# Performance work log

Hardware: AMD Instinct MI355X
Metric: run time of the kernel (lower is better)

## Reference

```python
import jax, jax.numpy as jnp
import numpy as np
import math

B, I, O, C = 8192, 1024, 1024, 6


def setup_inputs() -> dict:
    key = jax.random.key(0)
    k1, k2, k3, k4 = jax.random.split(key, 4)
    inputs = jax.random.normal(k1, (B, I), dtype=jnp.float32)
    phase_radians = jax.random.uniform(k2, (B,), dtype=jnp.float32) * (2.0 * math.pi)
    # xavier-uniform per control point: bound = sqrt(6/(I+O))
    bound = math.sqrt(6.0 / (I + O))
    weight_control_points = jax.random.uniform(k3, (C, O, I), dtype=jnp.float32, minval=-bound, maxval=bound)
    bias_control_points = jnp.zeros((C, O), dtype=jnp.float32) + 0.01 * jax.random.normal(k4, (C, O), dtype=jnp.float32)
    return {"inputs": inputs, "phase_radians": phase_radians,
            "weight_control_points": weight_control_points,
            "bias_control_points": bias_control_points}


def _catmull_rom(phase_radians, num_control_points):
    two_pi = 2.0 * math.pi
    phase = jnp.remainder(phase_radians, two_pi)
    position = phase * (float(num_control_points) / two_pi)
    base = jnp.floor(position)
    base_idx = base.astype(jnp.int32)
    t = position - base
    t2 = t * t
    t3 = t2 * t
    indices = jnp.stack([
        jnp.remainder(base_idx - 1, num_control_points),
        jnp.remainder(base_idx, num_control_points),
        jnp.remainder(base_idx + 1, num_control_points),
        jnp.remainder(base_idx + 2, num_control_points),
    ], axis=1)  # [B, 4]
    weights = jnp.stack([
        -0.5 * t + t2 - 0.5 * t3,
        1.0 - 2.5 * t2 + 1.5 * t3,
        0.5 * t + 2.0 * t2 - 1.5 * t3,
        -0.5 * t2 + 0.5 * t3,
    ], axis=1)  # [B, 4]
    return indices, weights


def reference(inputs, phase_radians, weight_control_points, bias_control_points):
    # Faithful to: out[b] = sum_k w[b,k] * (W[idx[b,k]] @ x[b] + bias[idx[b,k]])
    # Instead of materializing [B,O,I] interpolated weights, compute all C
    # control-point projections once and gather the 4 needed per sample.
    num_cp = weight_control_points.shape[0]
    indices, cr_weights = _catmull_rom(phase_radians.astype(inputs.dtype), num_cp)
    y_all = jnp.einsum('coi,bi->bco', weight_control_points, inputs)  # [B, C, O]
    y_sel = jnp.take_along_axis(y_all, indices[:, :, None], axis=1)  # [B, 4, O]
    b_sel = bias_control_points[indices]                              # [B, 4, O]
    return jnp.einsum('bk,bko->bo', cr_weights, y_sel + b_sel)
```

## Files before the change

kernel.cpp:

```cpp
#include <hip/hip_runtime.h>
#include <hip/hip_bf16.h>
#include <math.h>

#define B_SZ 8192
#define I_SZ 1024
#define O_SZ 1024
#define NCP  6

typedef __attribute__((ext_vector_type(8))) short bf16x8;
typedef __attribute__((ext_vector_type(4))) float f32x4;

__device__ __forceinline__ unsigned short f2bf(float f) {
  union { float f; unsigned int u; } v; v.f = f;
  unsigned int u = v.u;
  u += 0x7FFFu + ((u >> 16) & 1u);
  return (unsigned short)(u >> 16);
}

__global__ void cvt_f32_to_bf16(const float* __restrict__ src,
                                unsigned short* __restrict__ dst, int n4) {
  int idx = blockIdx.x * blockDim.x + threadIdx.x;
  int stride = gridDim.x * blockDim.x;
  for (int i = idx; i < n4; i += stride) {
    float4 v = reinterpret_cast<const float4*>(src)[i];
    ushort4 o;
    o.x = f2bf(v.x); o.y = f2bf(v.y); o.z = f2bf(v.z); o.w = f2bf(v.w);
    reinterpret_cast<ushort4*>(dst)[i] = o;
  }
}

__device__ __forceinline__ void gload_lds16(const void* g, void* l) {
  __builtin_amdgcn_global_load_lds(
      (const __attribute__((address_space(1))) void*)g,
      (__attribute__((address_space(3))) void*)l, 16, 0, 0);
}

#define BM 256
#define BN 128
#define BK 64
#define NT 96
#define NBUF 3

__global__ __launch_bounds__(512, 1) void pfl_gemm(
    const unsigned short* __restrict__ xb,
    const unsigned short* __restrict__ wb,
    const float* __restrict__ phase,
    const float* __restrict__ bias,
    float* __restrict__ out) {
  __shared__ __align__(16) unsigned short Abuf[NBUF][BM * BK];
  __shared__ __align__(16) unsigned short Bbuf[NBUF][BN * BK];
  __shared__ __align__(16) float c4[NCP][BM];

  const int nbn = O_SZ / BN;
  int bid = (int)blockIdx.x;
  int swz = (bid & 7) * 32 + (bid >> 3);
  int brow = (swz / nbn) * BM;
  int bcol = (swz % nbn) * BN;

  int tid = (int)threadIdx.x;
  int lane = tid & 63;
  int wid = tid >> 6;
  int wr = wid >> 1;
  int wc = wid & 1;

  if (tid < BM) {
    float ph = phase[brow + tid];
    const float two_pi = 6.2831855f;
    float pm = fmodf(ph, two_pi);
    float pos = pm * (float)(6.0 / 6.283185307179586);
    float base = floorf(pos);
    int bi = (int)base;
    float t = pos - base;
    float t2 = t * t, t3 = t2 * t;
    float w0 = -0.5f * t + t2 - 0.5f * t3;
    float w1 = 1.0f - 2.5f * t2 + 1.5f * t3;
    float w2 = 0.5f * t + 2.0f * t2 - 1.5f * t3;
    float w3 = -0.5f * t2 + 0.5f * t3;
    float cc[NCP] = {0.f, 0.f, 0.f, 0.f, 0.f, 0.f};
    cc[((bi - 1) % NCP + NCP) % NCP] += w0;
    cc[(bi % NCP + NCP) % NCP]       += w1;
    cc[((bi + 1) % NCP + NCP) % NCP] += w2;
    cc[((bi + 2) % NCP + NCP) % NCP] += w3;
    for (int j = 0; j < NCP; ++j) c4[j][tid] = cc[j];
  }

  f32x4 acc[4][4];
  f32x4 part[4][4];
#pragma unroll
  for (int m = 0; m < 4; ++m)
#pragma unroll
    for (int n = 0; n < 4; ++n) {
      acc[m][n] = (f32x4){0.f, 0.f, 0.f, 0.f};
      part[m][n] = (f32x4){0.f, 0.f, 0.f, 0.f};
    }

  int swzcol = ((lane & 7) ^ (lane >> 3)) * 8;
  const unsigned short* xsrc =
      xb + (size_t)(brow + wid * 8 + (lane >> 3)) * I_SZ + swzcol;
  const unsigned short* wsrc =
      wb + (size_t)(bcol + wid * 8 + (lane >> 3)) * I_SZ + swzcol;

  int lbase = (lane & 15) * 128 + (((lane >> 4) ^ (lane & 7)) & 7) * 16;

  auto STAGE = [&](int t, int b) {
    int ks = (t & 15) * 64;
    int j = t >> 4;
    const unsigned short* xs = xsrc + ks;
    const unsigned short* ws = wsrc + (size_t)j * O_SZ * I_SZ + ks;
    unsigned short* Ad = &Abuf[b][(wid * 8) * BK];
    unsigned short* Bd = &Bbuf[b][(wid * 8) * BK];
#pragma unroll
    for (int p = 0; p < 4; ++p)
      gload_lds16(xs + (size_t)p * 64 * I_SZ, Ad + p * 64 * BK);
#pragma unroll
    for (int p = 0; p < 2; ++p)
      gload_lds16(ws + (size_t)p * 64 * I_SZ, Bd + p * 64 * BK);
  };

  STAGE(0, 0);
  STAGE(1, 1);
  asm volatile("s_waitcnt vmcnt(6)" ::: "memory");
  __builtin_amdgcn_sched_barrier(0);
  __syncthreads();

  int cur = 0;
  for (int t = 0; t < NT; ++t) {
    const char* Ab = (const char*)&Abuf[cur][0];
    const char* Bb = (const char*)&Bbuf[cur][0];
    int st = cur + 2; if (st >= NBUF) st -= NBUF;

    bf16x8 af0[4], bf0[4], af1[4], bf1[4];
#pragma unroll
    for (int m = 0; m < 4; ++m)
      af0[m] = *reinterpret_cast<const bf16x8*>(
          Ab + (wr * 64 + m * 16) * 128 + lbase);
#pragma unroll
    for (int n = 0; n < 4; ++n)
      bf0[n] = *reinterpret_cast<const bf16x8*>(
          Bb + (wc * 64 + n * 16) * 128 + lbase);
    if (t + 2 < NT) STAGE(t + 2, st);
    asm volatile("s_waitcnt lgkmcnt(0)" ::: "memory");
    __builtin_amdgcn_sched_barrier(0);

#pragma unroll
    for (int m = 0; m < 4; ++m)
      af1[m] = *reinterpret_cast<const bf16x8*>(
          Ab + (wr * 64 + m * 16) * 128 + (lbase ^ 64));
#pragma unroll
    for (int n = 0; n < 4; ++n)
      bf1[n] = *reinterpret_cast<const bf16x8*>(
          Bb + (wc * 64 + n * 16) * 128 + (lbase ^ 64));
    __builtin_amdgcn_sched_barrier(0);

    __builtin_amdgcn_s_setprio(1);
#pragma unroll
    for (int m = 0; m < 4; ++m)
#pragma unroll
      for (int n = 0; n < 4; ++n)
        part[m][n] = __builtin_amdgcn_mfma_f32_16x16x32_bf16(
            af0[m], bf0[n], part[m][n], 0, 0, 0);
    __builtin_amdgcn_s_setprio(0);

    asm volatile("s_waitcnt lgkmcnt(0)" ::: "memory");
    __builtin_amdgcn_sched_barrier(0);

    __builtin_amdgcn_s_setprio(1);
#pragma unroll
    for (int m = 0; m < 4; ++m)
#pragma unroll
      for (int n = 0; n < 4; ++n)
        part[m][n] = __builtin_amdgcn_mfma_f32_16x16x32_bf16(
            af1[m], bf1[n], part[m][n], 0, 0, 0);
    __builtin_amdgcn_s_setprio(0);

    if ((t & 15) == 15) {
      int j = t >> 4;
#pragma unroll
      for (int m = 0; m < 4; ++m) {
        f32x4 cv = *reinterpret_cast<const f32x4*>(
            &c4[j][wr * 64 + m * 16 + (lane >> 4) * 4]);
#pragma unroll
        for (int n = 0; n < 4; ++n) {
          acc[m][n] += cv * part[m][n];
          part[m][n] = (f32x4){0.f, 0.f, 0.f, 0.f};
        }
      }
    }

    if (t + 2 < NT)
      asm volatile("s_waitcnt vmcnt(6)" ::: "memory");
    else
      asm volatile("s_waitcnt vmcnt(0)" ::: "memory");
    __builtin_amdgcn_sched_barrier(0);
    __builtin_amdgcn_s_barrier();
    ++cur; if (cur == NBUF) cur = 0;
  }

#pragma unroll
  for (int n = 0; n < 4; ++n) {
    int col = bcol + wc * 64 + n * 16 + (lane & 15);
    float b6[NCP];
#pragma unroll
    for (int j = 0; j < NCP; ++j) b6[j] = bias[j * O_SZ + col];
#pragma unroll
    for (int m = 0; m < 4; ++m) {
#pragma unroll
      for (int r = 0; r < 4; ++r) {
        int rloc = wr * 64 + m * 16 + (lane >> 4) * 4 + r;
        float s = 0.f;
#pragma unroll
        for (int j = 0; j < NCP; ++j) s += c4[j][rloc] * b6[j];
        out[(size_t)(brow + rloc) * O_SZ + col] = acc[m][n][r] + s;
      }
    }
  }
}

extern "C" void kernel_launch(void* const* d_in, const int* in_sizes, int n_in,
                              void* d_out, int out_size, void* d_ws, size_t ws_size,
                              hipStream_t stream) {
  (void)in_sizes; (void)n_in; (void)out_size; (void)ws_size;
  const float* x     = (const float*)d_in[0];
  const float* phase = (const float*)d_in[1];
  const float* w     = (const float*)d_in[2];
  const float* bias  = (const float*)d_in[3];
  float* out = (float*)d_out;

  unsigned short* xb = (unsigned short*)d_ws;
  unsigned short* wb = (unsigned short*)((char*)d_ws +
                        (size_t)B_SZ * I_SZ * sizeof(unsigned short));

  cvt_f32_to_bf16<<<2048, 256, 0, stream>>>(x, xb, B_SZ * I_SZ / 4);
  cvt_f32_to_bf16<<<1536, 256, 0, stream>>>(w, wb, NCP * O_SZ * I_SZ / 4);

  dim3 grid((B_SZ / BM) * (O_SZ / BN));
  pfl_gemm<<<grid, 512, 0, stream>>>(xb, wb, phase, bias, out);
}
```

Measured before the change: 123.2 us.

## Sort rows by spline segment to skip unused control-point GEMMs

Adds a single-block counting sort that groups batch rows by their Catmull-Rom base segment, then permutes and casts x into sorted order. Each 256-row block now loops only over the contiguous range of control points its rows actually need (typically 4 instead of 6), cutting MFMA work and weight traffic. Output rows are scattered back through the permutation. The cost is an extra serial sort kernel with an O(256) prefix loop per thread, a gather-based cast, and scattered output writes.

```diff
diff --git a/kernel.cpp b/kernel.cpp
--- a/kernel.cpp
+++ b/kernel.cpp
@@ -29,6 +29,78 @@
   }
 }
 
+__device__ __forceinline__ int seg_of(float ph) {
+  const float two_pi = 6.2831855f;
+  const float scale = (float)(6.0 / 6.283185307179586);
+  float pm = fmodf(ph, two_pi);
+  int bi = (int)floorf(pm * scale);
+  return ((bi % NCP) + NCP) % NCP;
+}
+
+__global__ void sort_rows(const float* __restrict__ phase,
+                          unsigned short* __restrict__ perm,
+                          int* __restrict__ blkinfo) {
+  __shared__ int hist[256][NCP];
+  __shared__ int segtot[NCP];
+  __shared__ int cum[NCP + 1];
+  __shared__ int thrbase[256][NCP];
+  int t = (int)threadIdx.x;
+  for (int s = 0; s < NCP; ++s) hist[t][s] = 0;
+  for (int i = 0; i < 32; ++i) {
+    int b = t * 32 + i;
+    hist[t][seg_of(phase[b])]++;
+  }
+  __syncthreads();
+  if (t < NCP) {
+    int tot = 0;
+    for (int tt = 0; tt < 256; ++tt) tot += hist[tt][t];
+    segtot[t] = tot;
+  }
+  __syncthreads();
+  if (t == 0) {
+    cum[0] = 0;
+    for (int s = 0; s < NCP; ++s) cum[s + 1] = cum[s] + segtot[s];
+  }
+  __syncthreads();
+  for (int s = 0; s < NCP; ++s) {
+    int p = 0;
+    for (int tt = 0; tt < t; ++tt) p += hist[tt][s];
+    thrbase[t][s] = cum[s] + p;
+  }
+  for (int i = 0; i < 32; ++i) {
+    int b = t * 32 + i;
+    int s = seg_of(phase[b]);
+    int pos = thrbase[t][s]++;
+    perm[pos] = (unsigned short)b;
+  }
+  __syncthreads();
+  if (t < B_SZ / 256) {
+    int start = t * 256, end = start + 255;
+    int s0 = 0; while (s0 < NCP - 1 && cum[s0 + 1] <= start) ++s0;
+    int s1 = 0; while (s1 < NCP - 1 && cum[s1 + 1] <= end) ++s1;
+    int nj = s1 - s0 + 4; if (nj > NCP) nj = NCP;
+    blkinfo[2 * t] = (s0 + NCP - 1) % NCP;
+    blkinfo[2 * t + 1] = nj;
+  }
+}
+
+__global__ void cast_x_perm(const float* __restrict__ x,
+                            const unsigned short* __restrict__ perm,
+                            unsigned short* __restrict__ xb) {
+  int idx = blockIdx.x * blockDim.x + threadIdx.x;
+  int stride = gridDim.x * blockDim.x;
+  const int total = B_SZ * (I_SZ / 4);
+  for (int i = idx; i < total; i += stride) {
+    int pos = i >> 8;
+    int c = i & 255;
+    int src = (int)perm[pos];
+    float4 v = reinterpret_cast<const float4*>(x + (size_t)src * I_SZ)[c];
+    ushort4 o;
+    o.x = f2bf(v.x); o.y = f2bf(v.y); o.z = f2bf(v.z); o.w = f2bf(v.w);
+    reinterpret_cast<ushort4*>(xb + (size_t)pos * I_SZ)[c] = o;
+  }
+}
+
 __device__ __forceinline__ void gload_lds16(const void* g, void* l) {
   __builtin_amdgcn_global_load_lds(
       (const __attribute__((address_space(1))) void*)g,
@@ -38,23 +110,26 @@
 #define BM 256
 #define BN 128
 #define BK 64
-#define NT 96
 #define NBUF 3
 
 __global__ __launch_bounds__(512, 1) void pfl_gemm(
     const unsigned short* __restrict__ xb,
     const unsigned short* __restrict__ wb,
     const float* __restrict__ phase,
+    const unsigned short* __restrict__ perm,
+    const int* __restrict__ blkinfo,
     const float* __restrict__ bias,
     float* __restrict__ out) {
   __shared__ __align__(16) unsigned short Abuf[NBUF][BM * BK];
   __shared__ __align__(16) unsigned short Bbuf[NBUF][BN * BK];
   __shared__ __align__(16) float c4[NCP][BM];
+  __shared__ int pblk[BM];
 
   const int nbn = O_SZ / BN;
   int bid = (int)blockIdx.x;
   int swz = (bid & 7) * 32 + (bid >> 3);
-  int brow = (swz / nbn) * BM;
+  int rowblk = swz / nbn;
+  int brow = rowblk * BM;
   int bcol = (swz % nbn) * BN;
 
   int tid = (int)threadIdx.x;
@@ -63,8 +138,13 @@
   int wr = wid >> 1;
   int wc = wid & 1;
 
+  int jlo = blkinfo[2 * rowblk];
+  int NTb = blkinfo[2 * rowblk + 1] << 4;
+
   if (tid < BM) {
-    float ph = phase[brow + tid];
+    int orow = (int)perm[brow + tid];
+    pblk[tid] = orow;
+    float ph = phase[orow];
     const float two_pi = 6.2831855f;
     float pm = fmodf(ph, two_pi);
     float pos = pm * (float)(6.0 / 6.283185307179586);
@@ -104,9 +184,9 @@
 
   auto STAGE = [&](int t, int b) {
     int ks = (t & 15) * 64;
-    int j = t >> 4;
+    int cN = jlo + (t >> 4); if (cN >= NCP) cN -= NCP;
     const unsigned short* xs = xsrc + ks;
-    const unsigned short* ws = wsrc + (size_t)j * O_SZ * I_SZ + ks;
+    const unsigned short* ws = wsrc + (size_t)cN * O_SZ * I_SZ + ks;
     unsigned short* Ad = &Abuf[b][(wid * 8) * BK];
     unsigned short* Bd = &Bbuf[b][(wid * 8) * BK];
 #pragma unroll
@@ -124,7 +204,7 @@
   __syncthreads();
 
   int cur = 0;
-  for (int t = 0; t < NT; ++t) {
+  for (int t = 0; t < NTb; ++t) {
     const char* Ab = (const char*)&Abuf[cur][0];
     const char* Bb = (const char*)&Bbuf[cur][0];
     int st = cur + 2; if (st >= NBUF) st -= NBUF;
@@ -138,7 +218,7 @@
     for (int n = 0; n < 4; ++n)
       bf0[n] = *reinterpret_cast<const bf16x8*>(
           Bb + (wc * 64 + n * 16) * 128 + lbase);
-    if (t + 2 < NT) STAGE(t + 2, st);
+    if (t + 2 < NTb) STAGE(t + 2, st);
     asm volatile("s_waitcnt lgkmcnt(0)" ::: "memory");
     __builtin_amdgcn_sched_barrier(0);
 
@@ -174,11 +254,11 @@
     __builtin_amdgcn_s_setprio(0);
 
     if ((t & 15) == 15) {
-      int j = t >> 4;
+      int cj = jlo + (t >> 4); if (cj >= NCP) cj -= NCP;
 #pragma unroll
       for (int m = 0; m < 4; ++m) {
         f32x4 cv = *reinterpret_cast<const f32x4*>(
-            &c4[j][wr * 64 + m * 16 + (lane >> 4) * 4]);
+            &c4[cj][wr * 64 + m * 16 + (lane >> 4) * 4]);
 #pragma unroll
         for (int n = 0; n < 4; ++n) {
           acc[m][n] += cv * part[m][n];
@@ -187,7 +267,7 @@
       }
     }
 
-    if (t + 2 < NT)
+    if (t + 2 < NTb)
       asm volatile("s_waitcnt vmcnt(6)" ::: "memory");
     else
       asm volatile("s_waitcnt vmcnt(0)" ::: "memory");
@@ -210,7 +290,7 @@
         float s = 0.f;
 #pragma unroll
         for (int j = 0; j < NCP; ++j) s += c4[j][rloc] * b6[j];
-        out[(size_t)(brow + rloc) * O_SZ + col] = acc[m][n][r] + s;
+        out[(size_t)pblk[rloc] * O_SZ + col] = acc[m][n][r] + s;
       }
     }
   }
@@ -226,13 +306,16 @@
   const float* bias  = (const float*)d_in[3];
   float* out = (float*)d_out;
 
-  unsigned short* xb = (unsigned short*)d_ws;
-  unsigned short* wb = (unsigned short*)((char*)d_ws +
-                        (size_t)B_SZ * I_SZ * sizeof(unsigned short));
-
-  cvt_f32_to_bf16<<<2048, 256, 0, stream>>>(x, xb, B_SZ * I_SZ / 4);
+  char* ws = (char*)d_ws;
+  unsigned short* xb = (unsigned short*)ws;
+  unsigned short* wb = (unsigned short*)(ws + (size_t)16 * 1024 * 1024);
+  unsigned short* perm = (unsigned short*)(ws + (size_t)28 * 1024 * 1024);
+  int* blkinfo = (int*)(ws + (size_t)28 * 1024 * 1024 + 16384);
+
+  sort_rows<<<1, 256, 0, stream>>>(phase, perm, blkinfo);
+  cast_x_perm<<<2048, 256, 0, stream>>>(x, perm, xb);
   cvt_f32_to_bf16<<<1536, 256, 0, stream>>>(w, wb, NCP * O_SZ * I_SZ / 4);
 
   dim3 grid((B_SZ / BM) * (O_SZ / BN));
-  pfl_gemm<<<grid, 512, 0, stream>>>(xb, wb, phase, bias, out);
-}
+  pfl_gemm<<<grid, 512, 0, stream>>>(xb, wb, phase, perm, blkinfo, bias, out);
+}
```

Result: slower. 136.1 us (+10.5%).
